# Kernel tuning notes

Hardware: AMD Instinct MI355X
Metric: run time of the kernel (lower is better)

The kernel has to match this reference:

```python
import jax, jax.numpy as jnp
import numpy as np

EMBED = 1024
HEADS = 16
HEAD_DIM = EMBED // HEADS
OUT = 1024


def setup_inputs() -> dict:
    key = jax.random.key(0)
    ks = jax.random.split(key, 6)
    x = jax.random.normal(ks[0], (4, 2048, EMBED), dtype=jnp.float32)
    # per-head projection weights, torch Linear convention: [out_features, in_features]
    s = 1.0 / np.sqrt(HEAD_DIM)
    Wv = jax.random.uniform(ks[1], (HEAD_DIM, HEAD_DIM), jnp.float32, -s, s)
    Wk = jax.random.uniform(ks[2], (HEAD_DIM, HEAD_DIM), jnp.float32, -s, s)
    Wq = jax.random.uniform(ks[3], (HEAD_DIM, HEAD_DIM), jnp.float32, -s, s)
    so = 1.0 / np.sqrt(EMBED)
    Wo = jax.random.uniform(ks[4], (OUT, EMBED), jnp.float32, -so, so)
    bo = jax.random.uniform(ks[5], (OUT,), jnp.float32, -so, so)
    return {"x": x, "Wq": Wq, "Wk": Wk, "Wv": Wv, "Wo": Wo, "bo": bo}


def reference(x, Wq, Wk, Wv, Wo, bo):
    N, L, _ = x.shape
    xh = x.reshape(N, L, HEADS, HEAD_DIM)  # nqhd
    q = jnp.einsum('nqhd,ed->nqhe', xh, Wq)
    k = jnp.einsum('nkhd,ed->nkhe', xh, Wk)
    v = jnp.einsum('nkhd,ed->nkhe', xh, Wv)
    # full score matrix [N, H, Q, K], scaled by sqrt(embed_size) as in source
    energy = jnp.einsum('nqhd,nkhd->nhqk', q, k) / np.sqrt(EMBED).astype(np.float32)
    attn = jax.nn.softmax(energy, axis=3)
    out = jnp.einsum('nhqk,nkhd->nqhd', attn, v).reshape(N, L, EMBED)
    return out @ Wo.T + bo
```

## Files before the change

kernel.cpp:

```cpp
#include <hip/hip_runtime.h>
#include <hip/hip_bf16.h>
#include <stdint.h>
#include <stddef.h>


typedef __attribute__((ext_vector_type(8))) short bf16x8;
typedef __attribute__((ext_vector_type(4))) float f32x4;
typedef __attribute__((ext_vector_type(4))) short short4v;
typedef __attribute__((ext_vector_type(2))) uint32_t uint2v;

__device__ __forceinline__ f32x4 mfma16(bf16x8 a, bf16x8 b, f32x4 c) {
    return __builtin_amdgcn_mfma_f32_16x16x32_bf16(a, b, c, 0, 0, 0);
}

__device__ __forceinline__ short f2bf(float x) {
    union { float f; uint32_t u; } v; v.f = x;
    uint32_t r = (v.u + 0x7FFFu + ((v.u >> 16) & 1u)) >> 16;
    return (short)(uint16_t)r;
}

__device__ __forceinline__ uint32_t pk2bf(float a, float b) {
    union { __hip_bfloat162 h; uint32_t u; } v;
    v.h = __float22bfloat162_rn(float2{a, b});
    return v.u;
}

__device__ __forceinline__ bf16x8 cvt8(const float* __restrict__ p) {
    f32x4 a = *(const f32x4*)p;
    f32x4 b = *(const f32x4*)(p + 4);
    bf16x8 r;
    r[0] = f2bf(a[0]); r[1] = f2bf(a[1]); r[2] = f2bf(a[2]); r[3] = f2bf(a[3]);
    r[4] = f2bf(b[0]); r[5] = f2bf(b[1]); r[6] = f2bf(b[2]); r[7] = f2bf(b[3]);
    return r;
}

__device__ __forceinline__ void swap16(uint32_t a, uint32_t b,
                                       uint32_t& lo, uint32_t& hi) {
#if __has_builtin(__builtin_amdgcn_permlane16_swap)
    uint2v r = __builtin_amdgcn_permlane16_swap(a, b, false, false);
    lo = r[0]; hi = r[1];
#else
    int lane = (int)(threadIdx.x & 63);
    uint32_t bl = (uint32_t)__shfl((int)b, lane & 47);
    uint32_t ah = (uint32_t)__shfl((int)a, lane | 16);
    lo = (lane & 16) ? bl : a;
    hi = (lane & 16) ? b : ah;
#endif
}

__global__ __launch_bounds__(256)
void wpack_kernel(const float* __restrict__ Wo, const float* __restrict__ Wq,
                  const float* __restrict__ Wk, const float* __restrict__ Wv,
                  short* __restrict__ wo_f, short* __restrict__ wqkv_f) {
    int b = blockIdx.x;
    if (b < 512) {
        int idx = b * 256 + threadIdx.x;
        int nrow = idx >> 7;
        int k0 = (idx & 127) * 8;
        bf16x8 v = cvt8(Wo + (size_t)nrow * 1024 + k0);
        int ntile = nrow >> 4, lcn = nrow & 15;
        int kseg = k0 >> 5, qd = (k0 >> 3) & 3;
        *(bf16x8*)(wo_f + ((size_t)(ntile * 32 + kseg) * 64 + qd * 16 + lcn) * 8) = v;
    } else {
        const float* W = (b == 512) ? Wq : (b == 513) ? Wk : Wv;
        short* dst = wqkv_f + (size_t)(b - 512) * 4096;
        for (int u = threadIdx.x; u < 512; u += 256) {
            int seg = u >> 6, ln = u & 63;
            int nt = seg >> 1, kf = seg & 1, lq = ln >> 4, lcn = ln & 15;
            bf16x8 v = cvt8(W + (nt * 16 + lcn) * 64 + kf * 32 + lq * 8);
            *(bf16x8*)(dst + u * 8) = v;
        }
    }
}

__global__ __launch_bounds__(256)
void kvproj_kernel(const float* __restrict__ x, const short* __restrict__ wqkv_f,
                   short* __restrict__ kf_ws, short* __restrict__ vf_ws) {
    __shared__ alignas(16) short kbuf[128 * 72];
    __shared__ alignas(16) short vbuf[64 * 136];
    int tid = threadIdx.x;
    int lt = blockIdx.x & 15, nh = blockIdx.x >> 4;
    int n = nh >> 4, h = nh & 15;
    int l0 = lt * 128, kt0 = lt * 2;
    int wv = tid >> 6, lane = tid & 63, quad = lane >> 4, lc = lane & 15;
    const short* wkf = wqkv_f + 4096 + lane * 8;
    const short* wvf = wqkv_f + 8192 + lane * 8;

    for (int u = tid; u < 1024; u += 256) {
        int r = u >> 3, c = (u & 7) * 8;
        *(bf16x8*)(kbuf + r * 72 + c) =
            cvt8(x + (size_t)(n * 2048 + l0 + r) * 1024 + h * 64 + c);
    }
    __syncthreads();

    bf16x8 xa[2][2];
    for (int mt = 0; mt < 2; ++mt)
        for (int kf = 0; kf < 2; ++kf)
            xa[mt][kf] = *(bf16x8*)(kbuf + (wv * 32 + mt * 16 + lc) * 72 + kf * 32 + quad * 8);

    f32x4 ka[2][4] = {}, va[2][4] = {};
    for (int nt = 0; nt < 4; ++nt)
        for (int kf = 0; kf < 2; ++kf) {
            bf16x8 wkb = *(const bf16x8*)(wkf + (nt * 2 + kf) * 512);
            bf16x8 wvb = *(const bf16x8*)(wvf + (nt * 2 + kf) * 512);
            for (int mt = 0; mt < 2; ++mt) {
                ka[mt][nt] = mfma16(xa[mt][kf], wkb, ka[mt][nt]);
                va[mt][nt] = mfma16(xa[mt][kf], wvb, va[mt][nt]);
            }
        }

    for (int mt = 0; mt < 2; ++mt) {
        int off = wv * 32 + mt * 16;
        for (int nt = 0; nt < 4; ++nt) {
            short4v pv;
            for (int i = 0; i < 4; ++i) {
                kbuf[(off + quad * 4 + i) * 72 + nt * 16 + lc] = f2bf(ka[mt][nt][i]);
                pv[i] = f2bf(va[mt][nt][i]);
            }
            *(short4v*)(vbuf + (nt * 16 + lc) * 136 + off + quad * 4) = pv;
        }
    }
    __syncthreads();

    size_t base = (size_t)nh * 131072 + (size_t)kt0 * 4096;
    for (int u = tid; u < 1024; u += 256) {
        int tile = u >> 9, rem = u & 511, seg = rem >> 6, ln = u & 63;
        int t = seg >> 1, kf = seg & 1;
        int lq = ln >> 4, ll = ln & 15;
        int bq = ((lq & 1) << 1) | (lq >> 1);
        bf16x8 kw = *(bf16x8*)(kbuf + (tile * 64 + t * 16 + ll) * 72 + kf * 32 + lq * 8);
        *(bf16x8*)(kf_ws + base + (size_t)tile * 4096 + seg * 512 + ln * 8) = kw;
        bf16x8 vw = *(bf16x8*)(vbuf + (t * 16 + ll) * 136 + tile * 64 + kf * 32 + bq * 8);
        *(bf16x8*)(vf_ws + base + (size_t)tile * 4096 + seg * 512 + ln * 8) = vw;
    }
}

__global__ __launch_bounds__(256, 4)
void flash_kernel(const float* __restrict__ x, const short* __restrict__ wqkv_f,
                  const short* __restrict__ kf_ws, const short* __restrict__ vf_ws,
                  short* __restrict__ ao) {
    __shared__ alignas(16) short pbuf[128 * 72];
    int tid = threadIdx.x;
    int nh = blockIdx.x & 63, qt = blockIdx.x >> 6;
    int n = nh >> 4, h = nh & 15;
    int q0 = qt * 128;
    int wv = tid >> 6, lane = tid & 63, quad = lane >> 4, lc = lane & 15;

    for (int u = tid; u < 1024; u += 256) {
        int r = u >> 3, c = (u & 7) * 8;
        *(bf16x8*)(pbuf + r * 72 + c) =
            cvt8(x + (size_t)(n * 2048 + q0 + r) * 1024 + h * 64 + c);
    }
    __syncthreads();
    {
        const short* wqf = wqkv_f + lane * 8;
        bf16x8 xa[2][2];
        for (int mt = 0; mt < 2; ++mt)
            for (int kf = 0; kf < 2; ++kf)
                xa[mt][kf] = *(bf16x8*)(pbuf + (wv * 32 + mt * 16 + lc) * 72 +
                                        kf * 32 + quad * 8);
        f32x4 qacc[2][4] = {};
        for (int nt = 0; nt < 4; ++nt)
            for (int kf = 0; kf < 2; ++kf) {
                bf16x8 wb = *(const bf16x8*)(wqf + (nt * 2 + kf) * 512);
                for (int mt = 0; mt < 2; ++mt)
                    qacc[mt][nt] = mfma16(xa[mt][kf], wb, qacc[mt][nt]);
            }
        const float QS = 0.04508422002778011f;
        for (int mt = 0; mt < 2; ++mt)
            for (int nt = 0; nt < 4; ++nt)
                for (int i = 0; i < 4; ++i)
                    pbuf[(wv * 32 + mt * 16 + quad * 4 + i) * 72 + nt * 16 + lc] =
                        f2bf(qacc[mt][nt][i] * QS);
    }
    __syncthreads();
    bf16x8 qa[2][2];
    for (int mt = 0; mt < 2; ++mt)
        for (int kf = 0; kf < 2; ++kf)
            qa[mt][kf] = *(bf16x8*)(pbuf + (wv * 32 + mt * 16 + lc) * 72 +
                                    kf * 32 + quad * 8);

    f32x4 o[2][4] = {};
    float lsum[2] = {0.f, 0.f};
    const short* kbase = kf_ws + (size_t)nh * 131072 + lane * 8;
    const short* vbase = vf_ws + (size_t)nh * 131072 + lane * 8;

    for (int kt = 0; kt < 32; ++kt) {
        const short* kp = kbase + (size_t)kt * 4096;
        const short* vp = vbase + (size_t)kt * 4096;
        bf16x8 kA[4][2], vA[4][2];
#pragma unroll
        for (int t = 0; t < 4; ++t)
            for (int kf = 0; kf < 2; ++kf) {
                kA[t][kf] = *(const bf16x8*)(kp + (t * 2 + kf) * 512);
                vA[t][kf] = *(const bf16x8*)(vp + (t * 2 + kf) * 512);
            }

#pragma unroll
        for (int q2 = 0; q2 < 2; ++q2) {
            f32x4 s[4];
#pragma unroll
            for (int t = 0; t < 4; ++t) {
                f32x4 acc = {};
                acc = mfma16(kA[t][0], qa[q2][0], acc);
                acc = mfma16(kA[t][1], qa[q2][1], acc);
                s[t] = acc;
            }
            uint32_t p0[4], p1[4];
            float ts = 0.f;
#pragma unroll
            for (int t = 0; t < 4; ++t) {
                float e0 = __builtin_amdgcn_exp2f(s[t][0]);
                float e1 = __builtin_amdgcn_exp2f(s[t][1]);
                float e2 = __builtin_amdgcn_exp2f(s[t][2]);
                float e3 = __builtin_amdgcn_exp2f(s[t][3]);
                ts += (e0 + e1) + (e2 + e3);
                p0[t] = pk2bf(e0, e1);
                p1[t] = pk2bf(e2, e3);
            }
            lsum[q2] += ts;
#pragma unroll
            for (int kf = 0; kf < 2; ++kf) {
                uint32_t r0, r1, r2, r3;
                swap16(p0[2 * kf], p0[2 * kf + 1], r0, r2);
                swap16(p1[2 * kf], p1[2 * kf + 1], r1, r3);
                union { uint32_t u[4]; bf16x8 v; } fr;
                fr.u[0] = r0; fr.u[1] = r1; fr.u[2] = r2; fr.u[3] = r3;
#pragma unroll
                for (int dt = 0; dt < 4; ++dt)
                    o[q2][dt] = mfma16(vA[dt][kf], fr.v, o[q2][dt]);
            }
        }
    }

    for (int q2 = 0; q2 < 2; ++q2) {
        float t = lsum[q2];
        t += __shfl_xor(t, 16, 64);
        t += __shfl_xor(t, 32, 64);
        float inv = 1.f / t;
        int mtile = (n * 2048 + q0) / 16 + wv * 2 + q2;
        for (int dt = 0; dt < 4; ++dt) {
            int kseg = h * 2 + (dt >> 1);
            int qd8 = ((dt & 1) * 4 + quad) >> 1;
            short4v pk;
            for (int i = 0; i < 4; ++i) pk[i] = f2bf(o[q2][dt][i] * inv);
            *(short4v*)(ao + (size_t)(mtile * 32 + kseg) * 512 +
                        (qd8 * 16 + lc) * 8 + (quad & 1) * 4) = pk;
        }
    }
}

__global__ __launch_bounds__(256)
void outgemm_kernel(const short* __restrict__ afb, const short* __restrict__ wfb,
                    const float* __restrict__ bo, float* __restrict__ out) {
    int tid = threadIdx.x;
    int bm = blockIdx.x & 63, bn = blockIdx.x >> 6;
    int m0 = bm * 128, n0 = bn * 128;
    int wv = tid >> 6, lane = tid & 63, quad = lane >> 4, lc = lane & 15;
    int wr = wv >> 1, wc = wv & 1;
    int mtb = bm * 8 + wr * 4;
    int ntb = bn * 8 + wc * 4;

    const short* ab = afb + lane * 8;
    const short* bb = wfb + lane * 8;

    f32x4 acc[4][4] = {};
    for (int kt = 0; kt < 32; ++kt) {
        bf16x8 af[4], bfr[4];
#pragma unroll
        for (int mt = 0; mt < 4; ++mt)
            af[mt] = *(const bf16x8*)(ab + ((size_t)(mtb + mt) * 32 + kt) * 512);
#pragma unroll
        for (int nt = 0; nt < 4; ++nt)
            bfr[nt] = *(const bf16x8*)(bb + ((size_t)(ntb + nt) * 32 + kt) * 512);
#pragma unroll
        for (int mt = 0; mt < 4; ++mt)
            for (int nt = 0; nt < 4; ++nt)
                acc[mt][nt] = mfma16(af[mt], bfr[nt], acc[mt][nt]);
    }
    for (int nt = 0; nt < 4; ++nt) {
        float bv = bo[n0 + wc * 64 + nt * 16 + lc];
        for (int mt = 0; mt < 4; ++mt)
            for (int i = 0; i < 4; ++i) {
                int m = m0 + wr * 64 + mt * 16 + quad * 4 + i;
                int nn = n0 + wc * 64 + nt * 16 + lc;
                out[(size_t)m * 1024 + nn] = acc[mt][nt][i] + bv;
            }
    }
}

extern "C" void kernel_launch(void* const* d_in, const int* in_sizes, int n_in,
                              void* d_out, int out_size, void* d_ws, size_t ws_size,
                              hipStream_t stream) {
    const float* x  = (const float*)d_in[0];
    const float* Wq = (const float*)d_in[1];
    const float* Wk = (const float*)d_in[2];
    const float* Wv = (const float*)d_in[3];
    const float* Wo = (const float*)d_in[4];
    const float* bo = (const float*)d_in[5];
    float* out = (float*)d_out;

    short* kf_ws   = (short*)d_ws;
    short* vf_ws   = kf_ws + 8388608;
    short* ao_ws   = vf_ws + 8388608;
    short* wo_f    = ao_ws + 8388608;
    short* wqkv_f  = wo_f + 1048576;

    wpack_kernel<<<dim3(515), dim3(256), 0, stream>>>(Wo, Wq, Wk, Wv, wo_f, wqkv_f);
    kvproj_kernel<<<dim3(1024), dim3(256), 0, stream>>>(x, wqkv_f, kf_ws, vf_ws);
    flash_kernel<<<dim3(1024), dim3(256), 0, stream>>>(x, wqkv_f, kf_ws, vf_ws, ao_ws);
    outgemm_kernel<<<dim3(512), dim3(256), 0, stream>>>(ao_ws, wo_f, bo, out);
}
```

Baseline: 206.3 us.

## Software-pipeline QK^T scores one key tile ahead in flash kernel

Restructures the flash attention loop so the scores for the next key tile are computed at the end of each iteration, overlapping the next tile's K loads and QK MFMAs with the current tile's exp and PV work. Launch bounds drop from 4 to 2 waves per SIMD so the extra live registers (next-tile K fragments and scores) fit. This trades occupancy for instruction-level overlap. The last iteration does a wasted wraparound load and QK compute.

```diff
diff --git a/kernel.cpp b/kernel.cpp
--- a/kernel.cpp
+++ b/kernel.cpp
@@ -135,7 +135,7 @@
     }
 }
 
-__global__ __launch_bounds__(256, 4)
+__global__ __launch_bounds__(256, 2)
 void flash_kernel(const float* __restrict__ x, const short* __restrict__ wqkv_f,
                   const short* __restrict__ kf_ws, const short* __restrict__ vf_ws,
                   short* __restrict__ ao) {
@@ -185,35 +185,45 @@
     const short* kbase = kf_ws + (size_t)nh * 131072 + lane * 8;
     const short* vbase = vf_ws + (size_t)nh * 131072 + lane * 8;
 
+    bf16x8 kN[4][2];
+    bf16x8 vA[4][2];
+    f32x4 s[2][4];
+
+#pragma unroll
+    for (int t = 0; t < 4; ++t)
+        for (int kf = 0; kf < 2; ++kf)
+            kN[t][kf] = *(const bf16x8*)(kbase + (t * 2 + kf) * 512);
+#pragma unroll
+    for (int q2 = 0; q2 < 2; ++q2)
+        for (int t = 0; t < 4; ++t) {
+            f32x4 acc = {};
+            acc = mfma16(kN[t][0], qa[q2][0], acc);
+            acc = mfma16(kN[t][1], qa[q2][1], acc);
+            s[q2][t] = acc;
+        }
+
     for (int kt = 0; kt < 32; ++kt) {
-        const short* kp = kbase + (size_t)kt * 4096;
         const short* vp = vbase + (size_t)kt * 4096;
-        bf16x8 kA[4][2], vA[4][2];
+        const short* kp = kbase + (size_t)((kt + 1) & 31) * 4096;
 #pragma unroll
         for (int t = 0; t < 4; ++t)
-            for (int kf = 0; kf < 2; ++kf) {
-                kA[t][kf] = *(const bf16x8*)(kp + (t * 2 + kf) * 512);
+            for (int kf = 0; kf < 2; ++kf)
                 vA[t][kf] = *(const bf16x8*)(vp + (t * 2 + kf) * 512);
-            }
+#pragma unroll
+        for (int t = 0; t < 4; ++t)
+            for (int kf = 0; kf < 2; ++kf)
+                kN[t][kf] = *(const bf16x8*)(kp + (t * 2 + kf) * 512);
 
 #pragma unroll
         for (int q2 = 0; q2 < 2; ++q2) {
-            f32x4 s[4];
-#pragma unroll
-            for (int t = 0; t < 4; ++t) {
-                f32x4 acc = {};
-                acc = mfma16(kA[t][0], qa[q2][0], acc);
-                acc = mfma16(kA[t][1], qa[q2][1], acc);
-                s[t] = acc;
-            }
             uint32_t p0[4], p1[4];
             float ts = 0.f;
 #pragma unroll
             for (int t = 0; t < 4; ++t) {
-                float e0 = __builtin_amdgcn_exp2f(s[t][0]);
-                float e1 = __builtin_amdgcn_exp2f(s[t][1]);
-                float e2 = __builtin_amdgcn_exp2f(s[t][2]);
-                float e3 = __builtin_amdgcn_exp2f(s[t][3]);
+                float e0 = __builtin_amdgcn_exp2f(s[q2][t][0]);
+                float e1 = __builtin_amdgcn_exp2f(s[q2][t][1]);
+                float e2 = __builtin_amdgcn_exp2f(s[q2][t][2]);
+                float e3 = __builtin_amdgcn_exp2f(s[q2][t][3]);
                 ts += (e0 + e1) + (e2 + e3);
                 p0[t] = pk2bf(e0, e1);
                 p1[t] = pk2bf(e2, e3);
@@ -231,6 +241,15 @@
                     o[q2][dt] = mfma16(vA[dt][kf], fr.v, o[q2][dt]);
             }
         }
+
+#pragma unroll
+        for (int q2 = 0; q2 < 2; ++q2)
+            for (int t = 0; t < 4; ++t) {
+                f32x4 acc = {};
+                acc = mfma16(kN[t][0], qa[q2][0], acc);
+                acc = mfma16(kN[t][1], qa[q2][1], acc);
+                s[q2][t] = acc;
+            }
     }
 
     for (int q2 = 0; q2 < 2; ++q2) {
```

New measurement: 233.3 us. 13.1% more time.
